# Kernel optimization log

Hardware: AMD Instinct MI355X
Metric: run time of the kernel (lower is better)

## Reference

```python
import jax, jax.numpy as jnp
import numpy as np

CONF_THRESH = 0.25


def setup_inputs() -> dict:
    key = jax.random.key(0)
    # Raw YOLO head output: [batch, n_anchors, 4 box + 1 objectness + 80 classes]
    output = jax.random.uniform(key, (16, 25200, 85), dtype=jnp.float32)
    return {"output": output}


def reference(output):
    # Faithful JAX version of ModelWrapper._process_raw_output fallback path.
    # Torch emits a variable-length [M, 6] tensor; with static shapes we emit
    # the dense [B, N, 6] decoded boxes with below-threshold rows zeroed
    # (equivalent information: masked rows are exactly the dropped ones).
    box_xy = output[..., 0:2]            # [B, N, 2]
    box_wh = output[..., 2:4]            # [B, N, 2]
    box_conf = output[..., 4]            # [B, N]
    box_cls = output[..., 5:]            # [B, N, C]

    half_wh = box_wh * 0.5
    xy_min = box_xy - half_wh            # xmin, ymin
    xy_max = box_xy + half_wh            # xmax, ymax

    max_scores = jnp.max(box_cls, axis=-1)                    # [B, N]
    max_cls_idx = jnp.argmax(box_cls, axis=-1)                # [B, N]
    scores = box_conf * max_scores                            # [B, N]
    mask = scores > CONF_THRESH                               # [B, N]

    boxes = jnp.concatenate(
        [xy_min, xy_max, scores[..., None],
         max_cls_idx.astype(output.dtype)[..., None]], axis=-1)  # [B, N, 6]
    return jnp.where(mask[..., None], boxes, jnp.zeros((), dtype=output.dtype))
```

## Files before the change

kernel.cpp:

```cpp
#include <hip/hip_runtime.h>

#define ROWS_PER_TILE 64
#define THREADS 64
#define ROW_F 85
#define NCLS 80
#define CONF_THRESH 0.25f

#define TILE_F (ROWS_PER_TILE * ROW_F)
#define TILE_V (TILE_F / 4)
#define PER_THREAD 21
#define TAIL_V (TILE_V - PER_THREAD * THREADS)
#define TILES_PER_BLOCK 8

#define GLOBAL_AS __attribute__((address_space(1)))
#define LDS_AS __attribute__((address_space(3)))

__global__ __launch_bounds__(THREADS) void yolo_post_kernel(
    const float* __restrict__ in, float* __restrict__ out, long long nrows) {
  __shared__ float tile[2][TILE_F];
  const int t = threadIdx.x;

  const long long full_tiles = nrows / ROWS_PER_TILE;
  const long long ntiles = (nrows + ROWS_PER_TILE - 1) / ROWS_PER_TILE;
  long long ti = (long long)blockIdx.x * TILES_PER_BLOCK;
  long long ti_end = ti + TILES_PER_BLOCK;
  if (ti_end > ntiles) ti_end = ntiles;
  if (ti >= ti_end) return;
  long long full_end = ti_end < full_tiles ? ti_end : full_tiles;

  auto stage = [&](int b, long long tt) {
    const float* src = in + tt * TILE_F;
#pragma unroll
    for (int k = 0; k < PER_THREAD; ++k) {
      __builtin_amdgcn_global_load_lds(
          (const GLOBAL_AS void*)(src + (long long)(t + k * THREADS) * 4),
          (LDS_AS void*)(&tile[b][k * THREADS * 4]), 16, 0, 0);
    }
    if (t < TAIL_V) {
      __builtin_amdgcn_global_load_lds(
          (const GLOBAL_AS void*)(src + (long long)(t + PER_THREAD * THREADS) * 4),
          (LDS_AS void*)(&tile[b][PER_THREAD * THREADS * 4]), 16, 0, 0);
    }
  };

  if (ti < full_end) {
    int cur = 0;
    stage(0, ti);
    for (; ti < full_end; ++ti) {
      __syncthreads();
      if (ti + 1 < full_end) stage(cur ^ 1, ti + 1);

      const long long r = ti * ROWS_PER_TILE + t;
      const float* row = &tile[cur][t * ROW_F];
      float cx = row[0];
      float cy = row[1];
      float hw = row[2] * 0.5f;
      float hh = row[3] * 0.5f;
      float conf = row[4];
      float best = row[5];
      int bidx = 0;
#pragma unroll
      for (int c = 1; c < NCLS; ++c) {
        float x = row[5 + c];
        bool g = x > best;
        best = g ? x : best;
        bidx = g ? c : bidx;
      }
      float score = conf * best;
      bool keep = score > CONF_THRESH;
      float2 o01 = keep ? make_float2(cx - hw, cy - hh) : make_float2(0.f, 0.f);
      float2 o23 = keep ? make_float2(cx + hw, cy + hh) : make_float2(0.f, 0.f);
      float2 o45 = keep ? make_float2(score, (float)bidx) : make_float2(0.f, 0.f);
      float2* op = (float2*)(out + r * 6);
      op[0] = o01;
      op[1] = o23;
      op[2] = o45;

      cur ^= 1;
    }
  }

  if (ti < ti_end) {
    const long long r = ti * ROWS_PER_TILE + t;
    if (r < nrows) {
      const float* __restrict__ row = in + r * ROW_F;
      float cx = row[0];
      float cy = row[1];
      float hw = row[2] * 0.5f;
      float hh = row[3] * 0.5f;
      float conf = row[4];
      float best = row[5];
      int bidx = 0;
      for (int c = 1; c < NCLS; ++c) {
        float x = row[5 + c];
        bool g = x > best;
        best = g ? x : best;
        bidx = g ? c : bidx;
      }
      float score = conf * best;
      bool keep = score > CONF_THRESH;
      float* op = out + r * 6;
      op[0] = keep ? cx - hw : 0.0f;
      op[1] = keep ? cy - hh : 0.0f;
      op[2] = keep ? cx + hw : 0.0f;
      op[3] = keep ? cy + hh : 0.0f;
      op[4] = keep ? score : 0.0f;
      op[5] = keep ? (float)bidx : 0.0f;
    }
  }
}

extern "C" void kernel_launch(void* const* d_in, const int* in_sizes, int n_in,
                              void* d_out, int out_size, void* d_ws, size_t ws_size,
                              hipStream_t stream) {
  const float* in = (const float*)d_in[0];
  float* out = (float*)d_out;
  const long long nrows = (long long)in_sizes[0] / ROW_F;
  const long long ntiles = (nrows + ROWS_PER_TILE - 1) / ROWS_PER_TILE;
  const int grid = (int)((ntiles + TILES_PER_BLOCK - 1) / TILES_PER_BLOCK);
  yolo_post_kernel<<<grid, THREADS, 0, stream>>>(in, out, nrows);
}
```

Before: 206.8 us.

## Split producer and consumer waves with triple-buffered LDS staging

Moves to 128-thread blocks in which wave 0 only issues async global-to-LDS loads and wave 1 only computes the argmax and writes output. Tiles are triple-buffered, with explicit vmcnt waits and raw s_barrier handoffs between the two waves, and each block now covers 13 tiles instead of 8. The goal is to keep loads in flight all the time and overlap them with compute, without every thread paying __syncthreads and load-issue cost. In exchange, the compute wave does all the arithmetic alone, LDS use per block grows, and correctness depends on the hand-counted waitcnt values and on the barrier counts matching between the waves.

```diff
diff --git a/kernel.cpp b/kernel.cpp
--- a/kernel.cpp
+++ b/kernel.cpp
@@ -1,87 +1,108 @@
 #include <hip/hip_runtime.h>
 
 #define ROWS_PER_TILE 64
-#define THREADS 64
 #define ROW_F 85
 #define NCLS 80
 #define CONF_THRESH 0.25f
-
 #define TILE_F (ROWS_PER_TILE * ROW_F)
-#define TILE_V (TILE_F / 4)
-#define PER_THREAD 21
-#define TAIL_V (TILE_V - PER_THREAD * THREADS)
-#define TILES_PER_BLOCK 8
+#define NBUF 3
+#define FULL_VEC 21
+#define TAIL_LANES 16
+#define VM_PER_TILE 22
+#define TILES_PER_BLOCK 13
+#define THREADS 128
 
 #define GLOBAL_AS __attribute__((address_space(1)))
 #define LDS_AS __attribute__((address_space(3)))
 
+#define WAITCNT_VM(n) (((n) & 0xF) | (((n) >> 4) << 14) | (0x7 << 4) | (0xF << 8))
+
 __global__ __launch_bounds__(THREADS) void yolo_post_kernel(
     const float* __restrict__ in, float* __restrict__ out, long long nrows) {
-  __shared__ float tile[2][TILE_F];
-  const int t = threadIdx.x;
+  __shared__ __align__(16) float tile[NBUF][TILE_F];
+
+  const int wave = threadIdx.x >> 6;
+  const int lane = threadIdx.x & 63;
 
   const long long full_tiles = nrows / ROWS_PER_TILE;
-  const long long ntiles = (nrows + ROWS_PER_TILE - 1) / ROWS_PER_TILE;
-  long long ti = (long long)blockIdx.x * TILES_PER_BLOCK;
-  long long ti_end = ti + TILES_PER_BLOCK;
-  if (ti_end > ntiles) ti_end = ntiles;
-  if (ti >= ti_end) return;
-  long long full_end = ti_end < full_tiles ? ti_end : full_tiles;
+  long long t0 = (long long)blockIdx.x * TILES_PER_BLOCK;
+  long long t1 = t0 + TILES_PER_BLOCK;
+  if (t1 > full_tiles) t1 = full_tiles;
+  const int nt = (int)(t1 > t0 ? t1 - t0 : 0);
 
-  auto stage = [&](int b, long long tt) {
-    const float* src = in + tt * TILE_F;
+  if (nt > 0) {
+    if (wave == 0) {
+      auto stage = [&](int b, long long tt) {
+        const float* src = in + tt * TILE_F;
 #pragma unroll
-    for (int k = 0; k < PER_THREAD; ++k) {
-      __builtin_amdgcn_global_load_lds(
-          (const GLOBAL_AS void*)(src + (long long)(t + k * THREADS) * 4),
-          (LDS_AS void*)(&tile[b][k * THREADS * 4]), 16, 0, 0);
-    }
-    if (t < TAIL_V) {
-      __builtin_amdgcn_global_load_lds(
-          (const GLOBAL_AS void*)(src + (long long)(t + PER_THREAD * THREADS) * 4),
-          (LDS_AS void*)(&tile[b][PER_THREAD * THREADS * 4]), 16, 0, 0);
-    }
-  };
+        for (int k = 0; k < FULL_VEC; ++k) {
+          __builtin_amdgcn_global_load_lds(
+              (const GLOBAL_AS void*)(src + (long long)(lane + k * 64) * 4),
+              (LDS_AS void*)(&tile[b][k * 256]), 16, 0, 0);
+        }
+        if (lane < TAIL_LANES) {
+          __builtin_amdgcn_global_load_lds(
+              (const GLOBAL_AS void*)(src + (long long)(lane + FULL_VEC * 64) * 4),
+              (LDS_AS void*)(&tile[b][FULL_VEC * 256]), 16, 0, 0);
+        }
+      };
 
-  if (ti < full_end) {
-    int cur = 0;
-    stage(0, ti);
-    for (; ti < full_end; ++ti) {
-      __syncthreads();
-      if (ti + 1 < full_end) stage(cur ^ 1, ti + 1);
+      stage(0, t0);
+      if (nt > 1) {
+        stage(1, t0 + 1);
+        __builtin_amdgcn_s_waitcnt(WAITCNT_VM(VM_PER_TILE));
+      } else {
+        __builtin_amdgcn_s_waitcnt(WAITCNT_VM(0));
+      }
+      __builtin_amdgcn_s_barrier();
+      for (int i = 0; i < nt; ++i) {
+        if (i + 2 < nt) stage((int)((i + 2) % NBUF), t0 + i + 2);
+        if (i + 1 < nt) {
+          if (i + 2 < nt)
+            __builtin_amdgcn_s_waitcnt(WAITCNT_VM(VM_PER_TILE));
+          else
+            __builtin_amdgcn_s_waitcnt(WAITCNT_VM(0));
+          __builtin_amdgcn_s_barrier();
+        }
+      }
+    } else {
+      __builtin_amdgcn_s_barrier();
+      for (int i = 0; i < nt; ++i) {
+        const long long tt = t0 + i;
+        const long long r = tt * ROWS_PER_TILE + lane;
+        const float* row = &tile[i % NBUF][lane * ROW_F];
 
-      const long long r = ti * ROWS_PER_TILE + t;
-      const float* row = &tile[cur][t * ROW_F];
-      float cx = row[0];
-      float cy = row[1];
-      float hw = row[2] * 0.5f;
-      float hh = row[3] * 0.5f;
-      float conf = row[4];
-      float best = row[5];
-      int bidx = 0;
+        float cx = row[0];
+        float cy = row[1];
+        float hw = row[2] * 0.5f;
+        float hh = row[3] * 0.5f;
+        float conf = row[4];
+        float best = row[5];
+        int bidx = 0;
 #pragma unroll
-      for (int c = 1; c < NCLS; ++c) {
-        float x = row[5 + c];
-        bool g = x > best;
-        best = g ? x : best;
-        bidx = g ? c : bidx;
+        for (int c = 1; c < NCLS; ++c) {
+          float x = row[5 + c];
+          bool g = x > best;
+          best = g ? x : best;
+          bidx = g ? c : bidx;
+        }
+        float score = conf * best;
+        bool keep = score > CONF_THRESH;
+        float2 o01 = keep ? make_float2(cx - hw, cy - hh) : make_float2(0.f, 0.f);
+        float2 o23 = keep ? make_float2(cx + hw, cy + hh) : make_float2(0.f, 0.f);
+        float2 o45 = keep ? make_float2(score, (float)bidx) : make_float2(0.f, 0.f);
+        float2* op = (float2*)(out + r * 6);
+        op[0] = o01;
+        op[1] = o23;
+        op[2] = o45;
+
+        if (i + 1 < nt) __builtin_amdgcn_s_barrier();
       }
-      float score = conf * best;
-      bool keep = score > CONF_THRESH;
-      float2 o01 = keep ? make_float2(cx - hw, cy - hh) : make_float2(0.f, 0.f);
-      float2 o23 = keep ? make_float2(cx + hw, cy + hh) : make_float2(0.f, 0.f);
-      float2 o45 = keep ? make_float2(score, (float)bidx) : make_float2(0.f, 0.f);
-      float2* op = (float2*)(out + r * 6);
-      op[0] = o01;
-      op[1] = o23;
-      op[2] = o45;
-
-      cur ^= 1;
     }
   }
 
-  if (ti < ti_end) {
-    const long long r = ti * ROWS_PER_TILE + t;
+  if (blockIdx.x == 0 && wave == 1) {
+    const long long r = full_tiles * ROWS_PER_TILE + lane;
     if (r < nrows) {
       const float* __restrict__ row = in + r * ROW_F;
       float cx = row[0];
@@ -116,7 +137,8 @@
   const float* in = (const float*)d_in[0];
   float* out = (float*)d_out;
   const long long nrows = (long long)in_sizes[0] / ROW_F;
-  const long long ntiles = (nrows + ROWS_PER_TILE - 1) / ROWS_PER_TILE;
-  const int grid = (int)((ntiles + TILES_PER_BLOCK - 1) / TILES_PER_BLOCK);
-  yolo_post_kernel<<<grid, THREADS, 0, stream>>>(in, out, nrows);
+  const long long full_tiles = nrows / ROWS_PER_TILE;
+  long long grid = (full_tiles + TILES_PER_BLOCK - 1) / TILES_PER_BLOCK;
+  if (grid < 1) grid = 1;
+  yolo_post_kernel<<<(int)grid, THREADS, 0, stream>>>(in, out, nrows);
 }
```

Result: faster. 194.9 us (-5.8%).
